# Kernel optimization log

Hardware: AMD Instinct MI355X
Metric: run time of the kernel (lower is better)

Reference implementation:

```python
import jax, jax.numpy as jnp
import numpy as np

N_USERS = 100000
N_ITEMS = 50000
N_NODES = N_USERS + N_ITEMS
EMBED = 64
NNZ = 4000000
BATCH = 4096
N_LAYERS = 3


def setup_inputs() -> dict:
    key = jax.random.key(0)
    k = jax.random.split(key, 8)
    return {
        "batch_user": jax.random.randint(k[0], (BATCH,), 0, N_USERS),
        "batch_pos_item": jax.random.randint(k[1], (BATCH,), 0, N_ITEMS),
        "batch_neg_item": jax.random.randint(k[2], (BATCH,), 0, N_ITEMS),
        "embed_user": jax.random.normal(k[3], (N_USERS, EMBED), dtype=jnp.float32) * 0.1,
        "embed_item": jax.random.normal(k[4], (N_ITEMS, EMBED), dtype=jnp.float32) * 0.1,
        "row_idx": jax.random.randint(k[5], (NNZ,), 0, N_NODES),
        "col_idx": jax.random.randint(k[6], (NNZ,), 0, N_NODES),
        "a_vals": jax.random.uniform(k[7], (NNZ,), dtype=jnp.float32),
    }


def reference(batch_user, batch_pos_item, batch_neg_item,
              embed_user, embed_item, row_idx, col_idx, a_vals):
    # E: [N_NODES, D] stacked user+item embeddings
    E = jnp.concatenate([embed_user, embed_item], axis=0)
    acc = E
    for _ in range(N_LAYERS):
        # SpMM in COO form: out[r] += a[e] * E[c[e]]
        msgs = a_vals[:, None] * E[col_idx]            # [NNZ, D]
        E = jax.ops.segment_sum(msgs, row_idx, num_segments=N_NODES)
        acc = acc + E
    out = acc / (N_LAYERS + 1)
    user_g = out[:N_USERS]
    item_g = out[N_USERS:]
    return (user_g[batch_user], item_g[batch_pos_item], item_g[batch_neg_item])
```

## Files before the change

kernel.cpp:

```cpp
#include <hip/hip_runtime.h>

#define N_USERS 100000
#define N_ITEMS 50000
#define N_NODES 150000
#define EMBED   64
#define NNZV    4000000
#define BATCH   4096
#define NBKT    293
#define CAP     16128

__global__ __launch_bounds__(512) void k_parta(
        const int* __restrict__ row, const int* __restrict__ col,
        const float* __restrict__ vals, int* __restrict__ bcnt,
        unsigned long long* __restrict__ staging, int nnz) {
    __shared__ int cnt[512];
    __shared__ int base_s[512];
    int tid = threadIdx.x;
    cnt[tid] = 0;
    __syncthreads();
    int tile0 = blockIdx.x * 16384;
    for (int k = 0; k < 32; k++) {
        int e = tile0 + k * 512 + tid;
        if (e < nnz) atomicAdd(&cnt[row[e] >> 9], 1);
    }
    __syncthreads();
    int c_ = cnt[tid];
    base_s[tid] = c_ ? (tid * CAP + atomicAdd(&bcnt[tid], c_)) : 0;
    __syncthreads();
    cnt[tid] = 0;
    __syncthreads();
    for (int k = 0; k < 32; k++) {
        int e = tile0 + k * 512 + tid;
        if (e < nnz) {
            int r = row[e];
            int b = r >> 9;
            int rank = atomicAdd(&cnt[b], 1);
            unsigned int key = ((unsigned int)(r & 511) << 18) | (unsigned int)col[e];
            unsigned long long rec = (unsigned long long)key
                                   | ((unsigned long long)__float_as_uint(vals[e]) << 32);
            staging[base_s[b] + rank] = rec;
        }
    }
}

__global__ __launch_bounds__(512) void k_partb(
        const int* __restrict__ bcnt,
        const unsigned long long* __restrict__ staging,
        int* __restrict__ row_ptr,
        unsigned long long* __restrict__ edges) {
    __shared__ int s[512];
    __shared__ int cnt[512];
    __shared__ int cur[512];
    __shared__ int base_sh;
    int b = blockIdx.x;
    int t = threadIdx.x;

    int v = (t < NBKT) ? bcnt[t] : 0;
    s[t] = v;
    __syncthreads();
    for (int off = 1; off < 512; off <<= 1) {
        int u = (t >= off) ? s[t - off] : 0;
        __syncthreads();
        s[t] += u;
        __syncthreads();
    }
    if (t == b) base_sh = s[t] - v;
    if (b == 0 && t == 0) row_ptr[N_NODES] = NNZV;
    __syncthreads();
    int base = base_sh;
    int n    = bcnt[b];
    const unsigned long long* sb = staging + (size_t)b * CAP;

    cnt[t] = 0;
    __syncthreads();
    for (int i = t; i < n; i += 512)
        atomicAdd(&cnt[(unsigned int)sb[i] >> 18], 1);
    __syncthreads();
    int c = cnt[t];
    s[t] = c;
    __syncthreads();
    for (int off = 1; off < 512; off <<= 1) {
        int u = (t >= off) ? s[t - off] : 0;
        __syncthreads();
        s[t] += u;
        __syncthreads();
    }
    int excl = s[t] - c;
    cur[t] = excl;
    int r = (b << 9) + t;
    if (r < N_NODES) row_ptr[r] = base + excl;
    __syncthreads();
    for (int i = t; i < n; i += 512) {
        unsigned long long rec = sb[i];
        unsigned int key = (unsigned int)rec;
        int rank = atomicAdd(&cur[key >> 18], 1);
        edges[base + rank] = (rec & 0xFFFFFFFF00000000ull) | (key & 0x3FFFFu);
    }
}

__device__ __forceinline__ float4 spmm_row(const int* row_ptr,
                                           const unsigned long long* edges,
                                           const float4* __restrict__ eu4,
                                           const float4* __restrict__ ei4s,
                                           int r, int lane) {
    int g = lane >> 4;
    int d = lane & 15;
    int start = row_ptr[r];
    int end   = row_ptr[r + 1];
    float4 acc = make_float4(0.f, 0.f, 0.f, 0.f);
    for (int e0 = start; e0 < end; e0 += 64) {
        int ei = e0 + lane;
        unsigned long long rec = 0ull;
        if (ei < end) rec = __builtin_nontemporal_load(edges + ei);
        int clo = (int)(rec & 0xffffffffull);
        int vhi = (int)(rec >> 32);
        int nleft = end - e0;
        int kmax = (nleft + 3) >> 2;
        #pragma unroll 4
        for (int k = 0; k < kmax; k++) {
            int src = 4 * k + g;
            int cc = __shfl(clo, src);
            float vv = __int_as_float(__shfl(vhi, src));
            const float4* basep = (cc < N_USERS) ? eu4 : ei4s;
            float4 e = basep[cc * 16 + d];
            acc.x += vv * e.x;
            acc.y += vv * e.y;
            acc.z += vv * e.z;
            acc.w += vv * e.w;
        }
    }
    acc.x += __shfl_xor(acc.x, 16);
    acc.y += __shfl_xor(acc.y, 16);
    acc.z += __shfl_xor(acc.z, 16);
    acc.w += __shfl_xor(acc.w, 16);
    acc.x += __shfl_xor(acc.x, 32);
    acc.y += __shfl_xor(acc.y, 32);
    acc.z += __shfl_xor(acc.z, 32);
    acc.w += __shfl_xor(acc.w, 32);
    return acc;
}

__global__ void k_spmm1(const int* __restrict__ row_ptr,
                        const unsigned long long* __restrict__ edges,
                        const float4* __restrict__ eu4,
                        const float4* __restrict__ ei4s,
                        float4* __restrict__ Eout) {
    int lane = threadIdx.x & 63;
    int r = blockIdx.x * 4 + (threadIdx.x >> 6);
    if (r >= N_NODES) return;
    float4 acc = spmm_row(row_ptr, edges, eu4, ei4s, r, lane);
    if (lane < 16) Eout[r * 16 + (lane & 15)] = acc;
}

__global__ void k_spmm(const int* __restrict__ row_ptr,
                       const unsigned long long* __restrict__ edges,
                       const float4* __restrict__ Ein,
                       float4* __restrict__ Eout) {
    int lane = threadIdx.x & 63;
    int r = blockIdx.x * 4 + (threadIdx.x >> 6);
    if (r >= N_NODES) return;
    float4 acc = spmm_row(row_ptr, edges, Ein, Ein, r, lane);
    if (lane < 16) Eout[r * 16 + (lane & 15)] = acc;
}

__global__ void k_spmm_batch(const int* __restrict__ row_ptr,
                             const unsigned long long* __restrict__ edges,
                             const float4* __restrict__ Ein,
                             const int* __restrict__ bu, const int* __restrict__ bp,
                             const int* __restrict__ bn,
                             float4* __restrict__ out) {
    int lane = threadIdx.x & 63;
    int j = blockIdx.x * 4 + (threadIdx.x >> 6);
    if (j >= 3 * BATCH) return;
    int r;
    if (j < BATCH)          r = bu[j];
    else if (j < 2 * BATCH) r = N_USERS + bp[j - BATCH];
    else                    r = N_USERS + bn[j - 2 * BATCH];
    float4 acc = spmm_row(row_ptr, edges, Ein, Ein, r, lane);
    if (lane < 16) {
        float4 e2 = Ein[r * 16 + lane];
        float4 o  = out[j * 16 + lane];
        o.x += 0.25f * (acc.x + e2.x);
        o.y += 0.25f * (acc.y + e2.y);
        o.z += 0.25f * (acc.z + e2.z);
        o.w += 0.25f * (acc.w + e2.w);
        out[j * 16 + lane] = o;
    }
}

__global__ void k_gather_init(const int* __restrict__ bu, const int* __restrict__ bp,
                              const int* __restrict__ bn,
                              const float4* __restrict__ eu4,
                              const float4* __restrict__ ei4s,
                              float4* __restrict__ out) {
    int idx = blockIdx.x * blockDim.x + threadIdx.x;
    if (idx >= 3 * BATCH * 16) return;
    int j = idx >> 4;
    int d = idx & 15;
    int node;
    if (j < BATCH)          node = bu[j];
    else if (j < 2 * BATCH) node = N_USERS + bp[j - BATCH];
    else                    node = N_USERS + bn[j - 2 * BATCH];
    const float4* basep = (node < N_USERS) ? eu4 : ei4s;
    float4 v = basep[node * 16 + d];
    v.x *= 0.25f; v.y *= 0.25f; v.z *= 0.25f; v.w *= 0.25f;
    out[idx] = v;
}

__global__ void k_gather_acc(const int* __restrict__ bu, const int* __restrict__ bp,
                             const int* __restrict__ bn, const float4* __restrict__ E,
                             float4* __restrict__ out) {
    int idx = blockIdx.x * blockDim.x + threadIdx.x;
    if (idx >= 3 * BATCH * 16) return;
    int j = idx >> 4;
    int d = idx & 15;
    int node;
    if (j < BATCH)          node = bu[j];
    else if (j < 2 * BATCH) node = N_USERS + bp[j - BATCH];
    else                    node = N_USERS + bn[j - 2 * BATCH];
    float4 v = E[node * 16 + d];
    float4 o = out[idx];
    o.x += 0.25f * v.x; o.y += 0.25f * v.y; o.z += 0.25f * v.z; o.w += 0.25f * v.w;
    out[idx] = o;
}

extern "C" void kernel_launch(void* const* d_in, const int* in_sizes, int n_in,
                              void* d_out, int out_size, void* d_ws, size_t ws_size,
                              hipStream_t stream) {
    const int*   bu   = (const int*)d_in[0];
    const int*   bp   = (const int*)d_in[1];
    const int*   bn   = (const int*)d_in[2];
    const float* eu   = (const float*)d_in[3];
    const float* ei   = (const float*)d_in[4];
    const int*   row  = (const int*)d_in[5];
    const int*   col  = (const int*)d_in[6];
    const float* vals = (const float*)d_in[7];
    float* out = (float*)d_out;

    char* p = (char*)d_ws;
    auto alloc = [&](size_t nbytes) {
        void* r = (void*)p;
        p += (nbytes + 255) & ~(size_t)255;
        return r;
    };
    float*              E_a     = (float*)alloc((size_t)N_NODES * EMBED * 4);
    float*              E_b     = (float*)alloc((size_t)N_NODES * EMBED * 4);
    unsigned long long* edges   = (unsigned long long*)alloc((size_t)NNZV * 8);
    int*                row_ptr = (int*)alloc((N_NODES + 1) * 4);
    int*                bcnt    = (int*)alloc(512 * 4);
    (void)ws_size; (void)n_in; (void)in_sizes; (void)out_size;

    unsigned long long* staging = (unsigned long long*)E_b;

    const float4* eu4  = (const float4*)eu;
    const float4* ei4s = (const float4*)ei - (size_t)N_USERS * 16;

    const int nnz = NNZV;
    hipMemsetAsync(bcnt, 0, 512 * sizeof(int), stream);

    k_parta<<<(nnz + 16383) / 16384, 512, 0, stream>>>(row, col, vals, bcnt, staging, nnz);
    k_partb<<<NBKT, 512, 0, stream>>>(bcnt, staging, row_ptr, edges);

    k_gather_init<<<(3 * BATCH * 16 + 255) / 256, 256, 0, stream>>>(
        bu, bp, bn, eu4, ei4s, (float4*)out);

    k_spmm1<<<(N_NODES + 3) / 4, 256, 0, stream>>>(row_ptr, edges, eu4, ei4s, (float4*)E_a);
    k_gather_acc<<<(3 * BATCH * 16 + 255) / 256, 256, 0, stream>>>(
        bu, bp, bn, (const float4*)E_a, (float4*)out);

    k_spmm<<<(N_NODES + 3) / 4, 256, 0, stream>>>(row_ptr, edges, (const float4*)E_a, (float4*)E_b);

    k_spmm_batch<<<(3 * BATCH + 3) / 4, 256, 0, stream>>>(
        row_ptr, edges, (const float4*)E_b, bu, bp, bn, (float4*)out);
}
```

Before: 516.5 us.

## Process four CSR rows per wavefront in SpMM with interleaved gathers

Replaces the one-row-per-wavefront SpMM kernels with a kernel where each 64-lane wavefront handles four consecutive rows and interleaves their edge loads and embedding gathers. Average row length is about 27 edges, so one row per wave leaves most of the 64 lanes idle during the edge load. Handling four rows at once gives more independent memory requests in flight. Edge records are read with nontemporal loads. The cost is higher register pressure from four float4 accumulators, and load imbalance because every row in the group iterates up to the longest row's length.

```diff
diff --git a/kernel.cpp b/kernel.cpp
--- a/kernel.cpp
+++ b/kernel.cpp
@@ -140,27 +140,81 @@
     return acc;
 }
 
-__global__ void k_spmm1(const int* __restrict__ row_ptr,
+__global__ void k_spmm4(const int* __restrict__ row_ptr,
                         const unsigned long long* __restrict__ edges,
                         const float4* __restrict__ eu4,
                         const float4* __restrict__ ei4s,
                         float4* __restrict__ Eout) {
     int lane = threadIdx.x & 63;
-    int r = blockIdx.x * 4 + (threadIdx.x >> 6);
-    if (r >= N_NODES) return;
-    float4 acc = spmm_row(row_ptr, edges, eu4, ei4s, r, lane);
-    if (lane < 16) Eout[r * 16 + (lane & 15)] = acc;
-}
-
-__global__ void k_spmm(const int* __restrict__ row_ptr,
-                       const unsigned long long* __restrict__ edges,
-                       const float4* __restrict__ Ein,
-                       float4* __restrict__ Eout) {
-    int lane = threadIdx.x & 63;
-    int r = blockIdx.x * 4 + (threadIdx.x >> 6);
-    if (r >= N_NODES) return;
-    float4 acc = spmm_row(row_ptr, edges, Ein, Ein, r, lane);
-    if (lane < 16) Eout[r * 16 + (lane & 15)] = acc;
+    int wv   = threadIdx.x >> 6;
+    int rbase = (blockIdx.x * 4 + wv) * 4;
+    if (rbase >= N_NODES) return;
+    int g = lane >> 4;
+    int d = lane & 15;
+    int st[4], en[4], len[4];
+    #pragma unroll
+    for (int i = 0; i < 4; i++) {
+        int r = rbase + i;
+        if (r < N_NODES) { st[i] = row_ptr[r]; en[i] = row_ptr[r + 1]; }
+        else             { st[i] = 0;          en[i] = 0; }
+        len[i] = en[i] - st[i];
+    }
+    int maxlen = len[0];
+    #pragma unroll
+    for (int i = 1; i < 4; i++) maxlen = (len[i] > maxlen) ? len[i] : maxlen;
+
+    float4 acc[4];
+    #pragma unroll
+    for (int i = 0; i < 4; i++) acc[i] = make_float4(0.f, 0.f, 0.f, 0.f);
+
+    for (int off = 0; off < maxlen; off += 64) {
+        int clo[4], vhi[4], kmax[4];
+        #pragma unroll
+        for (int i = 0; i < 4; i++) {
+            int ei = st[i] + off + lane;
+            unsigned long long rec = 0ull;
+            if (ei < en[i]) rec = __builtin_nontemporal_load(edges + ei);
+            clo[i] = (int)(rec & 0xffffffffull);
+            vhi[i] = (int)(rec >> 32);
+            int nleft = len[i] - off;
+            if (nleft < 0) nleft = 0; else if (nleft > 64) nleft = 64;
+            kmax[i] = (nleft + 3) >> 2;
+        }
+        int kmx = (maxlen - off + 3) >> 2; if (kmx > 16) kmx = 16;
+        #pragma unroll 4
+        for (int k = 0; k < kmx; k++) {
+            int src = 4 * k + g;
+            #pragma unroll
+            for (int i = 0; i < 4; i++) {
+                if (k < kmax[i]) {
+                    int cc = __shfl(clo[i], src);
+                    float vv = __int_as_float(__shfl(vhi[i], src));
+                    const float4* bp = (cc < N_USERS) ? eu4 : ei4s;
+                    float4 e = bp[cc * 16 + d];
+                    acc[i].x += vv * e.x;
+                    acc[i].y += vv * e.y;
+                    acc[i].z += vv * e.z;
+                    acc[i].w += vv * e.w;
+                }
+            }
+        }
+    }
+    #pragma unroll
+    for (int i = 0; i < 4; i++) {
+        acc[i].x += __shfl_xor(acc[i].x, 16);
+        acc[i].y += __shfl_xor(acc[i].y, 16);
+        acc[i].z += __shfl_xor(acc[i].z, 16);
+        acc[i].w += __shfl_xor(acc[i].w, 16);
+        acc[i].x += __shfl_xor(acc[i].x, 32);
+        acc[i].y += __shfl_xor(acc[i].y, 32);
+        acc[i].z += __shfl_xor(acc[i].z, 32);
+        acc[i].w += __shfl_xor(acc[i].w, 32);
+    }
+    if (lane < 16) {
+        #pragma unroll
+        for (int i = 0; i < 4; i++)
+            if (rbase + i < N_NODES) Eout[(rbase + i) * 16 + lane] = acc[i];
+    }
 }
 
 __global__ void k_spmm_batch(const int* __restrict__ row_ptr,
@@ -264,11 +318,15 @@
     k_gather_init<<<(3 * BATCH * 16 + 255) / 256, 256, 0, stream>>>(
         bu, bp, bn, eu4, ei4s, (float4*)out);
 
-    k_spmm1<<<(N_NODES + 3) / 4, 256, 0, stream>>>(row_ptr, edges, eu4, ei4s, (float4*)E_a);
+    k_spmm4<<<(N_NODES + 15) / 16, 256, 0, stream>>>(row_ptr, edges, eu4, ei4s,
+                                                     (float4*)E_a);
     k_gather_acc<<<(3 * BATCH * 16 + 255) / 256, 256, 0, stream>>>(
         bu, bp, bn, (const float4*)E_a, (float4*)out);
 
-    k_spmm<<<(N_NODES + 3) / 4, 256, 0, stream>>>(row_ptr, edges, (const float4*)E_a, (float4*)E_b);
+    k_spmm4<<<(N_NODES + 15) / 16, 256, 0, stream>>>(row_ptr, edges,
+                                                     (const float4*)E_a,
+                                                     (const float4*)E_a,
+                                                     (float4*)E_b);
 
     k_spmm_batch<<<(3 * BATCH + 3) / 4, 256, 0, stream>>>(
         row_ptr, edges, (const float4*)E_b, bu, bp, bn, (float4*)out);
```

After: 518.0 us. About the same (+0.3%).
